# Performance work log

Measured on AMD Instinct MI355X. Metric: run time of the kernel, lower is better.

Reference implementation:

```python
import jax, jax.numpy as jnp
import numpy as np
import math

N_HEADS = 8
N_LAYERS = 2
HYPER1 = 0.6
HYPER2 = 0.07


def setup_inputs() -> dict:
    key = jax.random.key(0)
    ks = jax.random.split(key, 32)
    B, S, D, M = 32, 512, 768, 384  # M = mem_dim = D // 2
    rn = lambda k, shape, scale: jax.random.normal(k, shape, jnp.float32) * scale
    sd, sm = 1.0 / math.sqrt(D), 1.0 / math.sqrt(M)
    inp = {
        'gcn_inputs': rn(ks[0], (B, S, D), 1.0),
        'adj_matrix': jax.random.uniform(ks[1], (B, S, S), jnp.float32),
        'attn_mask': jax.random.randint(ks[2], (B, 1, S), 0, 2).astype(jnp.int32),
        's_mask': jax.random.randint(ks[3], (B, S), 0, 2).astype(jnp.int32),
        'a_mask': jax.random.randint(ks[4], (B, S), 0, 2).astype(jnp.int32),
        # MultiHeadAttention: two Linear(d_model, d_model) for q and k
        'Wq': rn(ks[5], (D, D), sd), 'bq': jnp.zeros((D,), jnp.float32),
        'Wk': rn(ks[6], (D, D), sd), 'bk': jnp.zeros((D,), jnp.float32),
        # semW / depW: layer0 D->M, layer1 M->M
        'semW0': rn(ks[7], (D, M), sd), 'semb0': jnp.zeros((M,), jnp.float32),
        'semW1': rn(ks[8], (M, M), sm), 'semb1': jnp.zeros((M,), jnp.float32),
        'depW0': rn(ks[9], (D, M), sd), 'depb0': jnp.zeros((M,), jnp.float32),
        'depW1': rn(ks[10], (M, M), sm), 'depb1': jnp.zeros((M,), jnp.float32),
        # projection head fc1: M->32, fc2: 32->M
        'fc1W': rn(ks[11], (M, 32), sm), 'fc1b': jnp.zeros((32,), jnp.float32),
        'fc2W': rn(ks[12], (32, M), 1.0 / math.sqrt(32)), 'fc2b': jnp.zeros((M,), jnp.float32),
        # fc3: M->M, fc4: D->M
        'fc3W': rn(ks[13], (M, M), sm), 'fc3b': jnp.zeros((M,), jnp.float32),
        'fc4W': rn(ks[14], (D, M), sd), 'fc4b': jnp.zeros((M,), jnp.float32),
    }
    return inp


def _sim(z1, z2):
    # F.normalize(dim=2) then bmm
    n1 = z1 / jnp.maximum(jnp.linalg.norm(z1, axis=2, keepdims=True), 1e-12)
    n2 = z2 / jnp.maximum(jnp.linalg.norm(z2, axis=2, keepdims=True), 1e-12)
    return jnp.einsum('bsd,btd->bst', n1, n2)


def _diag(m):
    return jnp.diagonal(m, axis1=-2, axis2=-1)


def _scope_semi_loss(z1, z2, sm, am):
    f = lambda x: jnp.exp(x / HYPER2)
    a_z1 = z1 * am[..., None]
    m_between = f(_sim(a_z1, z2))
    m_refl = f(_sim(a_z1, z1))
    s_z1 = z1 * sm[..., None]
    s_z2 = z2 * sm[..., None]
    as_refl = f(_sim(a_z1, s_z1))
    as_between = f(_sim(a_z1, s_z2))
    w = _sim(a_z1, s_z2)
    weighted = f(w * _diag(w)[..., None])
    pos = (_diag(as_between)
           + (as_refl.sum(2) - _diag(as_refl))
           + (weighted.sum(2) - _diag(weighted)))
    alle = m_refl.sum(2) + m_between.sum(2) - _diag(m_refl)
    return -jnp.log(pos / alle)


def reference(gcn_inputs, adj_matrix, attn_mask, s_mask, a_mask,
              Wq, bq, Wk, bk,
              semW0, semb0, semW1, semb1,
              depW0, depb0, depW1, depb1,
              fc1W, fc1b, fc2W, fc2b, fc3W, fc3b, fc4W, fc4b):
    B, S, D = gcn_inputs.shape
    h, dk = N_HEADS, D // N_HEADS

    # ---- MultiHeadAttention -> per-head attention adjacency ----
    q = (gcn_inputs @ Wq + bq).reshape(B, S, h, dk).transpose(0, 2, 1, 3)
    k = (gcn_inputs @ Wk + bk).reshape(B, S, h, dk).transpose(0, 2, 1, 3)
    scores = jnp.einsum('bhsd,bhtd->bhst', q, k) / math.sqrt(dk)
    scores = jnp.where(attn_mask[:, None] == 0, -10000.0, scores)  # [B,1,1,S] broadcast
    attn = jax.nn.softmax(scores, axis=-1)  # dropout in eval mode -> identity

    # average heads, zero diagonal, add identity, row-mask by encoder atts
    adj_ag = attn.mean(axis=1)  # [B,S,S]
    eye = jnp.eye(S, dtype=adj_ag.dtype)
    adj_ag = adj_ag * (1.0 - eye) + eye
    atts = attn_mask.astype(adj_ag.dtype)  # text_encoder_atts [B,1,S]
    adj_ag = jnp.swapaxes(atts, 1, 2) * adj_ag

    # ---- gated dual-GCN layers ----
    sem_params = [(semW0, semb0), (semW1, semb1)]
    dep_params = [(depW0, depb0), (depW1, depb1)]
    H_l = gcn_inputs
    I_sem = None
    for l in range(N_LAYERS):
        sW, sb = sem_params[l]
        dW, db = dep_params[l]
        AH_sem = jnp.einsum('bst,btd->bsd', adj_ag, H_l)
        I_sem = AH_sem @ sW + sb
        AH_dep = jnp.einsum('bst,btd->bsd', adj_matrix, H_l)
        I_dep = AH_dep @ dW + db
        g = jax.nn.sigmoid(I_dep)
        I_dep_g = HYPER1 * g
        I_com = (1.0 - I_dep_g) * I_sem + I_dep_g * I_dep
        H_out = jax.nn.relu(I_com @ fc3W + fc3b)
        if l == 0:
            H_l = H_l @ fc4W + fc4b
        g_l = jax.nn.sigmoid(H_l)
        H_l = g_l * H_out + (1.0 - g_l) * H_l

    # ---- projection + symmetric contrastive scope loss ----
    proj = lambda z: jax.nn.elu(z @ fc1W + fc1b) @ fc2W + fc2b
    h1 = proj(H_l)
    h2 = proj(I_sem)
    smf = s_mask.astype(h1.dtype)
    amf = a_mask.astype(h1.dtype)
    l1 = _scope_semi_loss(h1, h2, smf, amf)
    l2 = _scope_semi_loss(h2, h1, smf, amf)
    loss = (l1 + l2) * 0.5
    loss_cl = loss.mean(axis=1, keepdims=True).mean()
    return loss_cl
```

## Files before the change

kernel.cpp:

```cpp
#include <hip/hip_runtime.h>
#include <math.h>


typedef __bf16 bf16x8 __attribute__((ext_vector_type(8)));
typedef __bf16 bf16x4 __attribute__((ext_vector_type(4)));
typedef float f32x4 __attribute__((ext_vector_type(4)));

__device__ __forceinline__ void glds16(const void* g, void* l) {
    __builtin_amdgcn_global_load_lds(
        (const __attribute__((address_space(1))) unsigned*)g,
        (__attribute__((address_space(3))) unsigned*)l, 16, 0, 0);
}

__device__ __forceinline__ float sigf(float x) { return 1.f / (1.f + __expf(-x)); }

__global__ __launch_bounds__(256) void mfma_gemm(
    const __bf16* __restrict__ A, const __bf16* __restrict__ B,
    const float* __restrict__ bias, int bzDiv, int bzStride,
    const __bf16* __restrict__ E,
    float* __restrict__ Cf, __bf16* __restrict__ Cb,
    int K, int lda, int ldb, int ldc, int nMax,
    long sAo, long sAi, long sBo, long sBi, int zInner, long sC, int act)
{
    __shared__ __bf16 As[2][128 * 32];
    __shared__ __bf16 Bs[2][128 * 32];
    int z = blockIdx.z;
    long aBase = (long)(z / zInner) * sAo + (long)(z % zInner) * sAi;
    long bBase = (long)(z / zInner) * sBo + (long)(z % zInner) * sBi;
    long cBase = (long)z * sC;
    int m0 = blockIdx.x * 128, n0 = blockIdx.y * 128;
    int tid = threadIdx.x;
    int wave = tid >> 6, lane = tid & 63;
    int wm = wave >> 1, wn = wave & 1;

    int e0 = tid, e1 = tid + 256;
    const __bf16* Ag0 = A + aBase + (long)(m0 + (e0 >> 2)) * lda + (e0 & 3) * 8;
    const __bf16* Ag1 = A + aBase + (long)(m0 + (e1 >> 2)) * lda + (e1 & 3) * 8;
    const __bf16* Bg0 = B + bBase + (long)(n0 + (e0 >> 2)) * ldb + (e0 & 3) * 8;
    const __bf16* Bg1 = B + bBase + (long)(n0 + (e1 >> 2)) * ldb + (e1 & 3) * 8;

    f32x4 acc[4][4];
#pragma unroll
    for (int i = 0; i < 4; i++)
#pragma unroll
        for (int j = 0; j < 4; j++) acc[i][j] = (f32x4){0.f, 0.f, 0.f, 0.f};

    int arow = wm * 64 + (lane & 15);
    int brow = wn * 64 + (lane & 15);
    int quad = lane >> 4;

    glds16(Ag0, As[0] + e0 * 8); glds16(Ag1, As[0] + e1 * 8);
    glds16(Bg0, Bs[0] + e0 * 8); glds16(Bg1, Bs[0] + e1 * 8);

    int cur = 0;
    for (int k0 = 0; k0 < K; k0 += 32) {
        __syncthreads();
        if (k0 + 32 < K) {
            int nk = k0 + 32, nb = cur ^ 1;
            glds16(Ag0 + nk, As[nb] + e0 * 8); glds16(Ag1 + nk, As[nb] + e1 * 8);
            glds16(Bg0 + nk, Bs[nb] + e0 * 8); glds16(Bg1 + nk, Bs[nb] + e1 * 8);
        }
        const bf16x8* Asv = (const bf16x8*)As[cur];
        const bf16x8* Bsv = (const bf16x8*)Bs[cur];
        bf16x8 af[4], bfr[4];
#pragma unroll
        for (int mi = 0; mi < 4; mi++) af[mi] = Asv[(arow + mi * 16) * 4 + quad];
#pragma unroll
        for (int ni = 0; ni < 4; ni++) bfr[ni] = Bsv[(brow + ni * 16) * 4 + quad];
#pragma unroll
        for (int mi = 0; mi < 4; mi++)
#pragma unroll
            for (int ni = 0; ni < 4; ni++)
                acc[mi][ni] = __builtin_amdgcn_mfma_f32_16x16x32_bf16(
                    af[mi], bfr[ni], acc[mi][ni], 0, 0, 0);
        cur ^= 1;
    }

    int crow = m0 + wm * 64 + (lane >> 4) * 4;
    int ccol = n0 + wn * 64 + (lane & 15);
    const float* biasz = bias ? bias + (z / bzDiv) * bzStride : nullptr;
    float bv[4];
#pragma unroll
    for (int ni = 0; ni < 4; ni++) {
        int col = ccol + ni * 16;
        bv[ni] = (biasz && col < nMax) ? biasz[col] : 0.f;
    }
#pragma unroll
    for (int mi = 0; mi < 4; mi++) {
#pragma unroll
        for (int ni = 0; ni < 4; ni++) {
            int col = ccol + ni * 16;
            if (col >= nMax) continue;
#pragma unroll
            for (int r = 0; r < 4; r++) {
                float v = acc[mi][ni][r] + bv[ni];
                long idx = cBase + (long)(crow + mi * 16 + r) * ldc + col;
                if (act == 1) v = fmaxf(v, 0.f);
                else if (act == 2) v = (v > 0.f) ? v : expm1f(v);
                else if (act == 4) {
                    float e = (float)E[idx];
                    v = fmaxf(v, 0.f);
                    float g = sigf(e);
                    v = g * v + (1.f - g) * e;
                }
                if (Cf) Cf[idx] = v;
                if (Cb) Cb[idx] = (__bf16)v;
            }
        }
    }
}

struct WCast {
    const float* src[10];
    unsigned dstOff[10];
    int R[10], C[10];
    int start[11];
};

__global__ __launch_bounds__(256) void castW_kernel(WCast wc, __bf16* wb)
{
    __shared__ float t[32][33];
    int bid = blockIdx.x;
    int e = 0;
    while (bid >= wc.start[e + 1]) e++;
    int tt = bid - wc.start[e];
    int cT = wc.C[e] >> 5;
    int ty = tt / cT, tx = tt - ty * cT;
    const float* in = wc.src[e];
    __bf16* out = wb + wc.dstOff[e];
    int R = wc.R[e], C = wc.C[e];
    int r0 = ty * 32, c0 = tx * 32;
    int tid = threadIdx.x;
    int r = tid >> 3, c4 = (tid & 7) * 4;
    float4 v = *(const float4*)(in + (long)(r0 + r) * C + c0 + c4);
    t[r][c4] = v.x; t[r][c4 + 1] = v.y; t[r][c4 + 2] = v.z; t[r][c4 + 3] = v.w;
    __syncthreads();
    int c = tid >> 3, r4 = (tid & 7) * 4;
    bf16x4 o;
    o[0] = (__bf16)t[r4 + 0][c]; o[1] = (__bf16)t[r4 + 1][c];
    o[2] = (__bf16)t[r4 + 2][c]; o[3] = (__bf16)t[r4 + 3][c];
    *(bf16x4*)(out + (long)(c0 + c) * R + r0 + r4) = o;
}

__global__ void cast_bf16_kernel(const float* __restrict__ in, __bf16* __restrict__ out, long n4)
{
    long i = (long)blockIdx.x * blockDim.x + threadIdx.x;
    if (i < n4) {
        float4 v = ((const float4*)in)[i];
        bf16x4 o; o[0] = (__bf16)v.x; o[1] = (__bf16)v.y; o[2] = (__bf16)v.z; o[3] = (__bf16)v.w;
        ((bf16x4*)out)[i] = o;
    }
}

__global__ __launch_bounds__(256) void softmax_combine(
    const __bf16* __restrict__ scores, const int* __restrict__ attn_mask,
    __bf16* __restrict__ adj_agb, int b0)
{
    const int S = 512;
    int s = blockIdx.x, bl = blockIdx.y, b = b0 + bl;
    int tid = threadIdx.x;
    const float scale = 0.1020620726159658f;
    int t0 = tid, t1 = tid + 256;
    int cm0 = attn_mask[b * S + t0], cm1 = attn_mask[b * S + t1];
    float vals[8][2], part[8];
#pragma unroll
    for (int h = 0; h < 8; ++h) {
        long rb = ((long)(bl * 8 + h) * S + s) * S;
        float r0 = (float)scores[rb + t0], r1 = (float)scores[rb + t1];
        vals[h][0] = cm0 ? __expf(r0 * scale) : 0.f;
        vals[h][1] = cm1 ? __expf(r1 * scale) : 0.f;
        part[h] = vals[h][0] + vals[h][1];
    }
    __shared__ float red[4][8];
    __shared__ float linv[8];
    int lane = tid & 63, w = tid >> 6;
#pragma unroll
    for (int h = 0; h < 8; ++h) {
        float v = part[h];
        for (int o = 32; o > 0; o >>= 1) v += __shfl_down(v, o);
        if (lane == 0) red[w][h] = v;
    }
    __syncthreads();
    if (tid < 8) {
        float l = red[0][tid] + red[1][tid] + red[2][tid] + red[3][tid];
        linv[tid] = 1.f / fmaxf(l, 1e-30f);
    }
    __syncthreads();
    float rowmask = attn_mask[b * S + s] ? 1.f : 0.f;
    float a0 = 0.f, a1 = 0.f;
#pragma unroll
    for (int h = 0; h < 8; ++h) { a0 += vals[h][0] * linv[h]; a1 += vals[h][1] * linv[h]; }
    a0 *= 0.125f; a1 *= 0.125f;
    if (t0 == s) a0 = 1.f;
    if (t1 == s) a1 = 1.f;
    long ob = ((long)b * S + s) * S;
    adj_agb[ob + t0] = (__bf16)(rowmask * a0);
    adj_agb[ob + t1] = (__bf16)(rowmask * a1);
}

__global__ void gcn_combine2(const __bf16* __restrict__ IsIdb,
                             __bf16* __restrict__ Icomb, long n8)
{
    long i = (long)blockIdx.x * blockDim.x + threadIdx.x;
    if (i >= n8) return;
    bf16x8 sv = ((const bf16x8*)IsIdb)[i];
    bf16x8 dv = ((const bf16x8*)(IsIdb + n8 * 8))[i];
    bf16x8 o;
#pragma unroll
    for (int j = 0; j < 8; j++) {
        float s = (float)sv[j], d = (float)dv[j];
        float g = 0.6f * sigf(d);
        o[j] = (__bf16)((1.f - g) * s + g * d);
    }
    ((bf16x8*)Icomb)[i] = o;
}

__global__ __launch_bounds__(128) void rownorm(__bf16* __restrict__ hb, int Dm)
{
    __bf16* p = hb + (long)blockIdx.x * Dm;
    int tid = threadIdx.x;
    float ss = 0.f;
    for (int i = tid; i < Dm; i += 128) { float v = (float)p[i]; ss += v * v; }
    for (int o = 32; o > 0; o >>= 1) ss += __shfl_down(ss, o);
    __shared__ float sb[2];
    __shared__ float scale;
    if ((tid & 63) == 0) sb[tid >> 6] = ss;
    __syncthreads();
    if (tid == 0) scale = 1.f / fmaxf(sqrtf(sb[0] + sb[1]), 1e-12f);
    __syncthreads();
    for (int i = tid; i < Dm; i += 128) p[i] = (__bf16)((float)p[i] * scale);
}

__global__ __launch_bounds__(256) void loss_kernel(
    const __bf16* __restrict__ G11, const __bf16* __restrict__ G12,
    const __bf16* __restrict__ G21, const __bf16* __restrict__ G22,
    const int* __restrict__ s_mask, const int* __restrict__ a_mask,
    float* __restrict__ lossb)
{
    const int S = 512;
    int s = blockIdx.x, b = blockIdx.y;
    int tid = threadIdx.x;
    if (a_mask[b * S + s] == 0) {
        if (tid == 0) lossb[b * S + s] = 0.f;
        return;
    }
    long base = ((long)b * S + s) * S;
    const float it = 1.f / 0.07f;
    float sms = s_mask[b * S + s] ? 1.f : 0.f;
    float d12 = (float)G12[base + s], d21 = (float)G21[base + s];
    float w1i = sms * d12 * it, w2i = sms * d21 * it;
    float p[8];
#pragma unroll
    for (int h = 0; h < 8; h++) p[h] = 0.f;
#pragma unroll
    for (int j = 0; j < 2; j++) {
        int t = tid + j * 256;
        bool smt = s_mask[b * S + t] != 0;
        bool off = (t != s);
        float g11 = (float)G11[base + t], g12 = (float)G12[base + t];
        float g21 = (float)G21[base + t], g22 = (float)G22[base + t];
        float e11 = __expf(g11 * it), e12 = __expf(g12 * it);
        float e21 = __expf(g21 * it), e22 = __expf(g22 * it);
        p[2] += e11; p[3] += e12; p[6] += e22; p[7] += e21;
        if (off) {
            p[0] += smt ? e11 : 1.f;
            p[4] += smt ? e22 : 1.f;
            p[1] += smt ? __expf(g12 * w1i) : 1.f;
            p[5] += smt ? __expf(g21 * w2i) : 1.f;
        }
    }
    __shared__ float red[4][8];
    int lane = tid & 63, w = tid >> 6;
#pragma unroll
    for (int h = 0; h < 8; h++) {
        float v = p[h];
        for (int o = 32; o > 0; o >>= 1) v += __shfl_down(v, o);
        if (lane == 0) red[w][h] = v;
    }
    __syncthreads();
    if (tid == 0) {
        float r[8];
#pragma unroll
        for (int h = 0; h < 8; h++) r[h] = red[0][h] + red[1][h] + red[2][h] + red[3][h];
        float g11ss = (float)G11[base + s], g22ss = (float)G22[base + s];
        float pos1 = __expf(w1i) + r[0] + r[1];
        float alle1 = r[2] - __expf(g11ss * it) + r[3];
        float pos2 = __expf(w2i) + r[4] + r[5];
        float alle2 = r[6] - __expf(g22ss * it) + r[7];
        lossb[b * S + s] = 0.5f * ((__logf(alle1) - __logf(pos1)) +
                                   (__logf(alle2) - __logf(pos2)));
    }
}

__global__ __launch_bounds__(256) void final_reduce(
    const float* __restrict__ lossb, float* __restrict__ out, int n)
{
    int tid = threadIdx.x;
    float s = 0.f;
    for (int i = tid; i < n; i += 256) s += lossb[i];
    for (int o = 32; o > 0; o >>= 1) s += __shfl_down(s, o);
    __shared__ float sb[4];
    if ((tid & 63) == 0) sb[tid >> 6] = s;
    __syncthreads();
    if (tid == 0) out[0] = (sb[0] + sb[1] + sb[2] + sb[3]) / (float)n;
}

static inline void mg(hipStream_t st, const __bf16* A, const __bf16* B,
                      const float* bias, int bzDiv, int bzStride,
                      const __bf16* E, float* Cf, __bf16* Cb,
                      int M, int Npad, int nMax, int K, int lda, int ldb, int ldc,
                      long sAo, long sAi, long sBo, long sBi, int zInner, long sC, int nz,
                      int act)
{
    dim3 g(M / 128, Npad / 128, nz);
    mfma_gemm<<<g, 256, 0, st>>>(A, B, bias, bzDiv, bzStride, E, Cf, Cb,
                                 K, lda, ldb, ldc, nMax,
                                 sAo, sAi, sBo, sBi, zInner, sC, act);
}

extern "C" void kernel_launch(void* const* d_in, const int* in_sizes, int n_in,
                              void* d_out, int out_size, void* d_ws, size_t ws_size,
                              hipStream_t stream)
{
    const int B = 32, S = 512, D = 768, Mm = 384;
    const int MT = B * S;
    const float* X    = (const float*)d_in[0];
    const float* adjm = (const float*)d_in[1];
    const int* attn_mask = (const int*)d_in[2];
    const int* s_mask    = (const int*)d_in[3];
    const int* a_mask    = (const int*)d_in[4];
    const float* Wq = (const float*)d_in[5],  *bq = (const float*)d_in[6];
    const float* Wk = (const float*)d_in[7],  *bk = (const float*)d_in[8];
    const float* semW0 = (const float*)d_in[9],  *semb0 = (const float*)d_in[10];
    const float* semW1 = (const float*)d_in[11], *semb1 = (const float*)d_in[12];
    const float* depW0 = (const float*)d_in[13], *depb0 = (const float*)d_in[14];
    const float* depW1 = (const float*)d_in[15], *depb1 = (const float*)d_in[16];
    const float* fc1W = (const float*)d_in[17], *fc1b = (const float*)d_in[18];
    const float* fc2W = (const float*)d_in[19], *fc2b = (const float*)d_in[20];
    const float* fc3W = (const float*)d_in[21], *fc3b = (const float*)d_in[22];
    const float* fc4W = (const float*)d_in[23], *fc4b = (const float*)d_in[24];

    char* ws = (char*)d_ws;
    const size_t MB = 1u << 20;
    const size_t KB = 1u << 10;

    __bf16* Xb      = (__bf16*)(ws + 0 * MB);
    __bf16* adj_agb = (__bf16*)(ws + 24 * MB);
    __bf16* adjmb   = (__bf16*)(ws + 40 * MB);
    __bf16* qkb     = (__bf16*)(ws + 56 * MB);
    __bf16* scoreB  = (__bf16*)(ws + 104 * MB);
    __bf16* P64     = (__bf16*)(ws + 56 * MB);
    __bf16* IsIdb   = (__bf16*)(ws + 80 * MB);
    __bf16* Isemb   = IsIdb;
    __bf16* Icomb   = (__bf16*)(ws + 104 * MB);
    __bf16* Hpreb   = (__bf16*)(ws + 116 * MB);
    __bf16* Hb      = (__bf16*)(ws + 128 * MB);
    __bf16* t1b     = (__bf16*)(ws + 0 * MB);
    __bf16* hb12    = (__bf16*)(ws + 140 * MB);
    __bf16* h1b     = hb12;
    __bf16* h2b     = hb12 + (long)MT * Mm;
    __bf16* G11     = (__bf16*)(ws + 24 * MB);
    __bf16* G12     = (__bf16*)(ws + 40 * MB);
    __bf16* G21     = (__bf16*)(ws + 56 * MB);
    __bf16* G22     = (__bf16*)(ws + 72 * MB);

    char* wreg = ws + 192 * MB;
    __bf16* wb     = (__bf16*)wreg;
    __bf16* WqkT   = (__bf16*)(wreg + 0 * KB);
    __bf16* semW0T = (__bf16*)(wreg + 2304 * KB);
    __bf16* depW0T = (__bf16*)(wreg + 2880 * KB);
    __bf16* fc4WT  = (__bf16*)(wreg + 3456 * KB);
    __bf16* semW1T = (__bf16*)(wreg + 4032 * KB);
    __bf16* depW1T = (__bf16*)(wreg + 4320 * KB);
    __bf16* fc3WT  = (__bf16*)(wreg + 4608 * KB);
    __bf16* fc1WT  = (__bf16*)(wreg + 4896 * KB);
    __bf16* fc2WT  = (__bf16*)(wreg + 4992 * KB);
    float*  bqk    = (float*)(wreg + 5016 * KB);
    float*  sbd0   = (float*)(wreg + 5024 * KB);
    float*  sbd1   = (float*)(wreg + 5028 * KB);
    float*  lossb  = (float*)(wreg + 5036 * KB);

    long nSM = (long)S * Mm, nSS = (long)S * S;
    long nPM = (long)Mm * S;

    cast_bf16_kernel<<<(MT * D / 4 + 255) / 256, 256, 0, stream>>>(X, Xb, (long)MT * D / 4);
    cast_bf16_kernel<<<((long)B * nSS / 4 + 255) / 256, 256, 0, stream>>>(adjm, adjmb, (long)B * nSS / 4);
    {
        WCast wc;
        const float* srcs[10] = {Wq, Wk, semW0, depW0, fc4W, semW1, depW1, fc3W, fc1W, fc2W};
        unsigned offs[10] = {0u, 589824u, 1179648u, 1474560u, 1769472u,
                             2064384u, 2211840u, 2359296u, 2506752u, 2555904u};
        int Rs[10] = {768, 768, 768, 768, 768, 384, 384, 384, 384, 32};
        int Cs[10] = {768, 768, 384, 384, 384, 384, 384, 384, 32, 384};
        int st = 0;
        for (int i = 0; i < 10; i++) {
            wc.src[i] = srcs[i]; wc.dstOff[i] = offs[i];
            wc.R[i] = Rs[i]; wc.C[i] = Cs[i];
            wc.start[i] = st; st += (Rs[i] / 32) * (Cs[i] / 32);
        }
        wc.start[10] = st;
        castW_kernel<<<st, 256, 0, stream>>>(wc, wb);
    }
    hipMemsetAsync(fc1WT + 32 * Mm, 0, (size_t)96 * Mm * 2, stream);
    hipMemcpyAsync(bqk, bq, D * 4, hipMemcpyDeviceToDevice, stream);
    hipMemcpyAsync(bqk + D, bk, D * 4, hipMemcpyDeviceToDevice, stream);
    hipMemcpyAsync(sbd0, semb0, Mm * 4, hipMemcpyDeviceToDevice, stream);
    hipMemcpyAsync(sbd0 + Mm, depb0, Mm * 4, hipMemcpyDeviceToDevice, stream);
    hipMemcpyAsync(sbd1, semb1, Mm * 4, hipMemcpyDeviceToDevice, stream);
    hipMemcpyAsync(sbd1 + Mm, depb1, Mm * 4, hipMemcpyDeviceToDevice, stream);

    mg(stream, Xb, WqkT, bqk, 1, 0, nullptr, nullptr, qkb, MT, 1536, 1536, D,
       D, D, 1536, 0, 0, 0, 0, 1, 0, 1, 0);

    for (int c = 0; c < 2; c++) {
        const __bf16* qc = qkb + (long)c * 16 * S * 1536;
        mg(stream, qc, qc + 768, nullptr, 1, 0, nullptr, nullptr, scoreB, S, S, S, 96,
           1536, 1536, S, (long)S * 1536, 96, (long)S * 1536, 96, 8, nSS, 128, 0);
        softmax_combine<<<dim3(S, 16), 256, 0, stream>>>(scoreB, attn_mask, adj_agb, c * 16);
    }

    long n8 = (long)MT * Mm / 8;
    int cwg = (int)((n8 + 255) / 256);

    mg(stream, semW0T, Xb, nullptr, 1, 0, nullptr, nullptr, P64, Mm, S, S, D,
       D, D, S, (long)Mm * D, 0, 0, (long)S * D, 32, nPM, 64, 0);
    mg(stream, adj_agb, P64, sbd0, 32, Mm, nullptr, nullptr, IsIdb, S, Mm, Mm, S,
       S, S, Mm, 0, nSS, 0, nPM, 64, nSM, 64, 0);
    gcn_combine2<<<cwg, 256, 0, stream>>>(IsIdb, Icomb, n8);
    mg(stream, Xb, fc4WT, fc4b, 1, 0, nullptr, nullptr, Hpreb, MT, Mm, Mm, D,
       D, D, Mm, 0, 0, 0, 0, 1, 0, 1, 0);
    mg(stream, Icomb, fc3WT, fc3b, 1, 0, Hpreb, nullptr, Hb, MT, Mm, Mm, Mm,
       Mm, Mm, Mm, 0, 0, 0, 0, 1, 0, 1, 4);

    mg(stream, semW1T, Hb, nullptr, 1, 0, nullptr, nullptr, P64, Mm, S, S, Mm,
       Mm, Mm, S, (long)Mm * Mm, 0, 0, nSM, 32, nPM, 64, 0);
    mg(stream, adj_agb, P64, sbd1, 32, Mm, nullptr, nullptr, IsIdb, S, Mm, Mm, S,
       S, S, Mm, 0, nSS, 0, nPM, 64, nSM, 64, 0);
    gcn_combine2<<<cwg, 256, 0, stream>>>(IsIdb, Icomb, n8);
    mg(stream, Icomb, fc3WT, fc3b, 1, 0, Hb, nullptr, Hb, MT, Mm, Mm, Mm,
       Mm, Mm, Mm, 0, 0, 0, 0, 1, 0, 1, 4);

    long sAproj = (long)(Isemb - Hb);
    mg(stream, Hb, fc1WT, fc1b, 1, 0, nullptr, nullptr, t1b, MT, 128, 32, Mm,
       Mm, Mm, 32, 0, sAproj, 0, 0, 2, (long)MT * 32, 2, 2);
    mg(stream, t1b, fc2WT, fc2b, 1, 0, nullptr, nullptr, hb12, MT, Mm, Mm, 32,
       32, 32, Mm, 0, (long)MT * 32, 0, 0, 2, (long)MT * Mm, 2, 0);

    rownorm<<<2 * MT, 128, 0, stream>>>(hb12, Mm);

    mg(stream, h1b, h1b, nullptr, 1, 0, nullptr, nullptr, G11, S, S, S, Mm,
       Mm, Mm, S, 0, nSM, 32 * nSM, nSM, 32, nSS, 64, 0);
    mg(stream, h2b, h1b, nullptr, 1, 0, nullptr, nullptr, G21, S, S, S, Mm,
       Mm, Mm, S, 0, nSM, 32 * nSM, nSM, 32, nSS, 64, 0);

    loss_kernel<<<dim3(S, B), 256, 0, stream>>>(G11, G12, G21, G22, s_mask, a_mask, lossb);
    final_reduce<<<1, 256, 0, stream>>>(lossb, (float*)d_out, MT);
}
```

Baseline: 802.8 us.

## Triple-buffer GEMM with swizzled LDS, grouped tile order, drop G21 via transpose

The GEMM kernel moves from double to triple-buffered LDS with explicit vmcnt waits, so global-to-LDS loads run two stages ahead. It also XOR-swizzles the LDS chunk layout to reduce bank conflicts, and remaps block indices into groups of 8 for better L2 reuse. In the loss stage, G21 is no longer computed; the kernel reads G12 transposed, using the fact that G21 is the transpose of G12, which saves one batched GEMM but makes those reads strided and uncoalesced. The Gram GEMM launch is also changed to write G22 with new strides, which may need checking against the other launches.

```diff
diff --git a/kernel.cpp b/kernel.cpp
--- a/kernel.cpp
+++ b/kernel.cpp
@@ -22,22 +22,35 @@
     int K, int lda, int ldb, int ldc, int nMax,
     long sAo, long sAi, long sBo, long sBi, int zInner, long sC, int act)
 {
-    __shared__ __bf16 As[2][128 * 32];
-    __shared__ __bf16 Bs[2][128 * 32];
+    __shared__ __bf16 As[3][128 * 32];
+    __shared__ __bf16 Bs[3][128 * 32];
     int z = blockIdx.z;
+
+    int gx = gridDim.x, gy = gridDim.y;
+    int lin = blockIdx.x + gx * blockIdx.y;
+    const int GRP = 8;
+    int per = GRP * gy;
+    int grp = lin / per, rr = lin - grp * per;
+    int x0 = grp * GRP;
+    int width = (gx - x0 < GRP) ? (gx - x0) : GRP;
+    int bx = x0 + rr % width, by = rr / width;
+
     long aBase = (long)(z / zInner) * sAo + (long)(z % zInner) * sAi;
     long bBase = (long)(z / zInner) * sBo + (long)(z % zInner) * sBi;
     long cBase = (long)z * sC;
-    int m0 = blockIdx.x * 128, n0 = blockIdx.y * 128;
+    int m0 = bx * 128, n0 = by * 128;
     int tid = threadIdx.x;
     int wave = tid >> 6, lane = tid & 63;
     int wm = wave >> 1, wn = wave & 1;
 
     int e0 = tid, e1 = tid + 256;
-    const __bf16* Ag0 = A + aBase + (long)(m0 + (e0 >> 2)) * lda + (e0 & 3) * 8;
-    const __bf16* Ag1 = A + aBase + (long)(m0 + (e1 >> 2)) * lda + (e1 & 3) * 8;
-    const __bf16* Bg0 = B + bBase + (long)(n0 + (e0 >> 2)) * ldb + (e0 & 3) * 8;
-    const __bf16* Bg1 = B + bBase + (long)(n0 + (e1 >> 2)) * ldb + (e1 & 3) * 8;
+    int r0 = e0 >> 2, r1 = e1 >> 2;
+    int q0 = (e0 & 3) ^ (r0 & 3) ^ ((r0 >> 2) & 3);
+    int q1 = (e1 & 3) ^ (r1 & 3) ^ ((r1 >> 2) & 3);
+    const __bf16* Ag0 = A + aBase + (long)(m0 + r0) * lda + q0 * 8;
+    const __bf16* Ag1 = A + aBase + (long)(m0 + r1) * lda + q1 * 8;
+    const __bf16* Bg0 = B + bBase + (long)(n0 + r0) * ldb + q0 * 8;
+    const __bf16* Bg1 = B + bBase + (long)(n0 + r1) * ldb + q1 * 8;
 
     f32x4 acc[4][4];
 #pragma unroll
@@ -45,35 +58,46 @@
 #pragma unroll
         for (int j = 0; j < 4; j++) acc[i][j] = (f32x4){0.f, 0.f, 0.f, 0.f};
 
-    int arow = wm * 64 + (lane & 15);
-    int brow = wn * 64 + (lane & 15);
+    int rl = lane & 15;
     int quad = lane >> 4;
-
+    int qs = quad ^ (rl & 3) ^ ((rl >> 2) & 3);
+    int arow = wm * 64 + rl;
+    int brow = wn * 64 + rl;
+
+    int nk = K >> 5;
     glds16(Ag0, As[0] + e0 * 8); glds16(Ag1, As[0] + e1 * 8);
     glds16(Bg0, Bs[0] + e0 * 8); glds16(Bg1, Bs[0] + e1 * 8);
-
-    int cur = 0;
-    for (int k0 = 0; k0 < K; k0 += 32) {
-        __syncthreads();
-        if (k0 + 32 < K) {
-            int nk = k0 + 32, nb = cur ^ 1;
-            glds16(Ag0 + nk, As[nb] + e0 * 8); glds16(Ag1 + nk, As[nb] + e1 * 8);
-            glds16(Bg0 + nk, Bs[nb] + e0 * 8); glds16(Bg1 + nk, Bs[nb] + e1 * 8);
+    if (nk > 1) {
+        glds16(Ag0 + 32, As[1] + e0 * 8); glds16(Ag1 + 32, As[1] + e1 * 8);
+        glds16(Bg0 + 32, Bs[1] + e0 * 8); glds16(Bg1 + 32, Bs[1] + e1 * 8);
+    }
+
+    int bi = 0;
+    for (int i = 0; i < nk; ++i) {
+        __builtin_amdgcn_sched_barrier(0);
+        if (i + 1 < nk) asm volatile("s_waitcnt vmcnt(4) lgkmcnt(0)" ::: "memory");
+        else            asm volatile("s_waitcnt vmcnt(0) lgkmcnt(0)" ::: "memory");
+        __builtin_amdgcn_s_barrier();
+        if (i + 2 < nk) {
+            int pb = bi + 2; if (pb >= 3) pb -= 3;
+            int ko = (i + 2) * 32;
+            glds16(Ag0 + ko, As[pb] + e0 * 8); glds16(Ag1 + ko, As[pb] + e1 * 8);
+            glds16(Bg0 + ko, Bs[pb] + e0 * 8); glds16(Bg1 + ko, Bs[pb] + e1 * 8);
         }
-        const bf16x8* Asv = (const bf16x8*)As[cur];
-        const bf16x8* Bsv = (const bf16x8*)Bs[cur];
+        const bf16x8* Asv = (const bf16x8*)As[bi];
+        const bf16x8* Bsv = (const bf16x8*)Bs[bi];
         bf16x8 af[4], bfr[4];
 #pragma unroll
-        for (int mi = 0; mi < 4; mi++) af[mi] = Asv[(arow + mi * 16) * 4 + quad];
-#pragma unroll
-        for (int ni = 0; ni < 4; ni++) bfr[ni] = Bsv[(brow + ni * 16) * 4 + quad];
+        for (int mi = 0; mi < 4; mi++) af[mi] = Asv[(arow + mi * 16) * 4 + qs];
+#pragma unroll
+        for (int ni = 0; ni < 4; ni++) bfr[ni] = Bsv[(brow + ni * 16) * 4 + qs];
 #pragma unroll
         for (int mi = 0; mi < 4; mi++)
 #pragma unroll
             for (int ni = 0; ni < 4; ni++)
                 acc[mi][ni] = __builtin_amdgcn_mfma_f32_16x16x32_bf16(
                     af[mi], bfr[ni], acc[mi][ni], 0, 0, 0);
-        cur ^= 1;
+        bi++; if (bi >= 3) bi -= 3;
     }
 
     int crow = m0 + wm * 64 + (lane >> 4) * 4;
@@ -233,7 +257,7 @@
 
 __global__ __launch_bounds__(256) void loss_kernel(
     const __bf16* __restrict__ G11, const __bf16* __restrict__ G12,
-    const __bf16* __restrict__ G21, const __bf16* __restrict__ G22,
+    const __bf16* __restrict__ G22,
     const int* __restrict__ s_mask, const int* __restrict__ a_mask,
     float* __restrict__ lossb)
 {
@@ -245,10 +269,11 @@
         return;
     }
     long base = ((long)b * S + s) * S;
+    long cbase = (long)b * S * S + s;
     const float it = 1.f / 0.07f;
     float sms = s_mask[b * S + s] ? 1.f : 0.f;
-    float d12 = (float)G12[base + s], d21 = (float)G21[base + s];
-    float w1i = sms * d12 * it, w2i = sms * d21 * it;
+    float d12 = (float)G12[base + s];
+    float w1i = sms * d12 * it, w2i = w1i;
     float p[8];
 #pragma unroll
     for (int h = 0; h < 8; h++) p[h] = 0.f;
@@ -258,7 +283,8 @@
         bool smt = s_mask[b * S + t] != 0;
         bool off = (t != s);
         float g11 = (float)G11[base + t], g12 = (float)G12[base + t];
-        float g21 = (float)G21[base + t], g22 = (float)G22[base + t];
+        float g21 = (float)G12[cbase + (long)t * S];
+        float g22 = (float)G22[base + t];
         float e11 = __expf(g11 * it), e12 = __expf(g12 * it);
         float e21 = __expf(g21 * it), e22 = __expf(g22 * it);
         p[2] += e11; p[3] += e12; p[6] += e22; p[7] += e21;
@@ -361,7 +387,6 @@
     __bf16* h2b     = hb12 + (long)MT * Mm;
     __bf16* G11     = (__bf16*)(ws + 24 * MB);
     __bf16* G12     = (__bf16*)(ws + 40 * MB);
-    __bf16* G21     = (__bf16*)(ws + 56 * MB);
     __bf16* G22     = (__bf16*)(ws + 72 * MB);
 
     char* wreg = ws + 192 * MB;
@@ -450,9 +475,9 @@
 
     mg(stream, h1b, h1b, nullptr, 1, 0, nullptr, nullptr, G11, S, S, S, Mm,
        Mm, Mm, S, 0, nSM, 32 * nSM, nSM, 32, nSS, 64, 0);
-    mg(stream, h2b, h1b, nullptr, 1, 0, nullptr, nullptr, G21, S, S, S, Mm,
-       Mm, Mm, S, 0, nSM, 32 * nSM, nSM, 32, nSS, 64, 0);
-
-    loss_kernel<<<dim3(S, B), 256, 0, stream>>>(G11, G12, G21, G22, s_mask, a_mask, lossb);
+    mg(stream, h2b, h2b, nullptr, 1, 0, nullptr, nullptr, G22, S, S, S, Mm,
+       Mm, Mm, S, 0, nSM, 0, nSM, 32, nSS, 32, 0);
+
+    loss_kernel<<<dim3(S, B), 256, 0, stream>>>(G11, G12, G22, s_mask, a_mask, lossb);
     final_reduce<<<1, 256, 0, stream>>>(lossb, (float*)d_out, MT);
 }
```

New measurement: 803.6 us. Within noise of the previous version (+0.1%).
